# Optimization experiments

Measured on AMD Instinct MI355X. Metric: run time of the kernel, lower is better.

The kernel has to match this reference:

```python
import jax, jax.numpy as jnp
import numpy as np

N_NODES = 100_000
N_EDGES = 1_600_000
IN_DIM, HIDDEN, Z_DIM = 64, 128, 64


def _gcn_conv(x, src, dst, dinv, W, b, n):
    # PyG GCNConv: out_i = sum_j (d_i^-1/2 d_j^-1/2) (x_j @ W) + b, edges incl. self-loops
    xw = x @ W                                   # [N, out]
    norm = dinv[src] * dinv[dst]                 # [E+N]
    msg = xw[src] * norm[:, None]                # [E+N, out]
    return jax.ops.segment_sum(msg, dst, num_segments=n) + b


def _prep_graph(edge_index, n):
    loop = jnp.arange(n, dtype=edge_index.dtype)
    src = jnp.concatenate([edge_index[0], loop])
    dst = jnp.concatenate([edge_index[1], loop])
    deg = jax.ops.segment_sum(jnp.ones_like(dst, dtype=jnp.float32), dst, num_segments=n)
    dinv = jnp.where(deg > 0, jax.lax.rsqrt(jnp.maximum(deg, 1.0)), 0.0)
    return src, dst, dinv


def setup_inputs() -> dict:
    key = jax.random.key(0)
    ks = jax.random.split(key, 8)
    x = jax.random.normal(ks[0], (N_NODES, IN_DIM), dtype=jnp.float32)
    edge_index = jax.random.randint(ks[1], (2, N_EDGES), 0, N_NODES, dtype=jnp.int32)

    def glorot(k, fi, fo):
        s = (6.0 / (fi + fo)) ** 0.5
        return jax.random.uniform(k, (fi, fo), jnp.float32, -s, s)

    return {
        "x": x, "edge_index": edge_index,
        "W1": glorot(ks[2], IN_DIM, HIDDEN), "b1": jnp.zeros((HIDDEN,), jnp.float32),
        "W2": glorot(ks[3], HIDDEN, HIDDEN), "b2": jnp.zeros((HIDDEN,), jnp.float32),
        "Wmu": glorot(ks[4], HIDDEN, Z_DIM), "bmu": jnp.zeros((Z_DIM,), jnp.float32),
        "Wlv": glorot(ks[5], HIDDEN, Z_DIM), "blv": jnp.zeros((Z_DIM,), jnp.float32),
    }


def reference(x, edge_index, W1, b1, W2, b2, Wmu, bmu, Wlv, blv):
    n = x.shape[0]
    src, dst, dinv = _prep_graph(edge_index, n)
    h = jax.nn.relu(_gcn_conv(x, src, dst, dinv, W1, b1, n))
    h = jax.nn.relu(_gcn_conv(h, src, dst, dinv, W2, b2, n))
    # dropout p=0.0 (eval): identity
    mu = _gcn_conv(h, src, dst, dinv, Wmu, bmu, n)
    logvar = _gcn_conv(h, src, dst, dinv, Wlv, blv, n)
    return (mu, logvar)
```

## Files before the change

### kernel.cpp

```cpp
#include <hip/hip_runtime.h>
#include <hip/hip_fp16.h>
#include <cstddef>

#define N_NODES 100000
#define N_EDGES 1600000
#define E_TOT   (N_EDGES + N_NODES)
#define IN_DIM  64
#define HIDDEN  128
#define Z_DIM   64

#define BN 128
#define NB ((N_NODES + BN - 1) / BN)
#define NCH 128

using f16x8 = __attribute__((ext_vector_type(8))) _Float16;
using f32x4 = __attribute__((ext_vector_type(4))) float;


__global__ __launch_bounds__(256) void prep_k(const float* __restrict__ x, __half* __restrict__ x16,
                                              const float* __restrict__ W1, const float* __restrict__ W2,
                                              const float* __restrict__ Wmu, const float* __restrict__ Wlv,
                                              __half* __restrict__ W1t, __half* __restrict__ W2t,
                                              __half* __restrict__ Wht) {
    int i = blockIdx.x * 256 + threadIdx.x;
    const int CAST = N_NODES * IN_DIM / 8;
    if (i < CAST) {
        const float4* in4 = (const float4*)x;
        float4 a = in4[2 * i], b = in4[2 * i + 1];
        __half2 h0 = __floats2half2_rn(a.x, a.y);
        __half2 h1 = __floats2half2_rn(a.z, a.w);
        __half2 h2 = __floats2half2_rn(b.x, b.y);
        __half2 h3 = __floats2half2_rn(b.z, b.w);
        uint4 pk = make_uint4(*(unsigned*)&h0, *(unsigned*)&h1, *(unsigned*)&h2, *(unsigned*)&h3);
        ((uint4*)x16)[i] = pk;
        return;
    }
    int j = i - CAST;
    if (j < 128 * 64) {
        int col = j >> 6, k = j & 63;
        W1t[j] = __float2half(W1[k * 128 + col]);
        return;
    }
    int m = j - 128 * 64;
    if (m < 128 * 128) {
        int col = m >> 7, k = m & 127;
        W2t[m] = __float2half(W2[k * 128 + col]);
        return;
    }
    int h = m - 128 * 128;
    if (h < 128 * 128) {
        int col = h >> 7, k = h & 127;
        Wht[h] = __float2half(col < 64 ? Wmu[k * 64 + col] : Wlv[k * 64 + (col - 64)]);
    }
}


__global__ __launch_bounds__(256) void hist_k(const int* __restrict__ dst, int* __restrict__ histG, int e) {
    __shared__ int hist[NB];
    int c = blockIdx.x, t = threadIdx.x;
    int ch = (e + NCH - 1) / NCH;
    int i0 = c * ch, i1 = i0 + ch; if (i1 > e) i1 = e;
    for (int b = t; b < NB; b += 256) hist[b] = 0;
    __syncthreads();
    for (int i = i0 + t; i < i1; i += 256)
        atomicAdd(&hist[dst[i] >> 7], 1);
    __syncthreads();
    for (int b = t; b < NB; b += 256) histG[c * NB + b] = hist[b];
}

__global__ __launch_bounds__(1024) void boff_k(int* __restrict__ histG ,
                                               int* __restrict__ ebase, int e) {
    __shared__ int s[1024];
    int t = threadIdx.x;
    int run = 0;
    if (t < NB) {
        for (int c = 0; c < NCH; c++) {
            int v = histG[c * NB + t];
            histG[c * NB + t] = run;
            run += v;
        }
    }
    s[t] = (t < NB) ? run : 0;
    __syncthreads();
#pragma unroll
    for (int off = 1; off < 1024; off <<= 1) {
        int x = (t >= off) ? s[t - off] : 0;
        __syncthreads();
        s[t] += x;
        __syncthreads();
    }
    if (t < NB) ebase[t] = s[t] - run;
    if (t == 0) ebase[NB] = e;
}

__global__ __launch_bounds__(256) void binB_k(const int* __restrict__ src, const int* __restrict__ dst,
                                              const int* __restrict__ boffs, const int* __restrict__ ebase,
                                              int* __restrict__ binned, int e) {
    __shared__ int cur[NB];
    int c = blockIdx.x, t = threadIdx.x;
    int ch = (e + NCH - 1) / NCH;
    int i0 = c * ch, i1 = i0 + ch; if (i1 > e) i1 = e;
    for (int b = t; b < NB; b += 256) cur[b] = ebase[b] + boffs[c * NB + b];
    __syncthreads();
    for (int i = i0 + t; i < i1; i += 256) {
        int s = src[i], d = dst[i];
        int p = atomicAdd(&cur[d >> 7], 1);
        binned[p] = ((d & 127) << 17) | s;
    }
}

__global__ __launch_bounds__(256) void pdeg_k(const int* __restrict__ binned, const int* __restrict__ ebase,
                                              int* __restrict__ rowptr, float* __restrict__ dinv, int n) {
    __shared__ int hist[BN];
    __shared__ int sc[BN];
    int b = blockIdx.x, t = threadIdx.x;
    int n0 = b * BN;
    int nn = n - n0; if (nn > BN) nn = BN;
    if (t < BN) hist[t] = (t < nn) ? 1 : 0;
    __syncthreads();
    int e0 = ebase[b], e1 = ebase[b + 1];
    for (int i = e0 + t; i < e1; i += 256)
        atomicAdd(&hist[binned[i] >> 17], 1);
    __syncthreads();
    int v = (t < BN) ? hist[t] : 0;
    if (t < BN) sc[t] = v;
    __syncthreads();
#pragma unroll
    for (int off = 1; off < BN; off <<= 1) {
        int x = (t < BN && t >= off) ? sc[t - off] : 0;
        __syncthreads();
        if (t < BN) sc[t] += x;
        __syncthreads();
    }
    int base = e0 + n0;
    if (t < nn) {
        rowptr[n0 + t] = base + sc[t] - v;
        dinv[n0 + t] = rsqrtf((float)v);
    }
    if (b == gridDim.x - 1 && t == 0) rowptr[n] = E_TOT;
}

__global__ __launch_bounds__(256) void pfill_k(const int* __restrict__ binned, const int* __restrict__ ebase,
                                               const int* __restrict__ rowptr, const float* __restrict__ dinv,
                                               int2* __restrict__ em, int n) {
    __shared__ int cur[BN];
    __shared__ float sdv[BN];
    int b = blockIdx.x, t = threadIdx.x;
    int n0 = b * BN;
    int nn = n - n0; if (nn > BN) nn = BN;
    if (t < nn) {
        int rp = rowptr[n0 + t];
        float dv = dinv[n0 + t];
        sdv[t] = dv;
        em[rp] = make_int2(n0 + t, __float_as_int(dv * dv));
        cur[t] = rp + 1;
    }
    __syncthreads();
    int e0 = ebase[b], e1 = ebase[b + 1];
    for (int i = e0 + t; i < e1; i += 256) {
        int pk = binned[i];
        int ld = pk >> 17, s = pk & 0x1FFFF;
        int q = atomicAdd(&cur[ld], 1);
        em[q] = make_int2(s, __float_as_int(dinv[s] * sdv[ld]));
    }
}


template <int DIM, bool HEAD>
__global__ __launch_bounds__(256) void agg_k(const __half* __restrict__ H, const int* __restrict__ rowptr,
                                             const int2* __restrict__ em, __half* __restrict__ out,
                                             const float* __restrict__ bmu, const float* __restrict__ blv,
                                             float* __restrict__ mu, float* __restrict__ lv, int n) {
    int node = (int)((blockIdx.x * 256 + threadIdx.x) >> 6);
    if (node >= n) return;
    int lane = threadIdx.x & 63;
    int beg = rowptr[node], end = rowptr[node + 1];
    const uint4* H4 = (const uint4*)H;

    constexpr int RV   = DIM / 8;
    constexpr int SUBS = 64 / RV;
    constexpr int STEP = SUBS * 2;
    int sub = lane / RV;
    int fl  = lane % RV;

    float acc[8];
#pragma unroll
    for (int q = 0; q < 8; q++) acc[q] = 0.f;

    auto meta = [&](int j, int p, int& s, float& w) {
        int idx = j + SUBS * p + sub;
        int ci  = idx < end ? idx : beg;
        int2 e  = em[ci];
        s = e.x;
        w = idx < end ? __int_as_float(e.y) : 0.f;
    };
    auto rows = [&](int s0, int s1, uint4& r0, uint4& r1) {
        r0 = H4[(size_t)s0 * RV + fl];
        r1 = H4[(size_t)s1 * RV + fl];
    };
    auto fmas = [&](const uint4& r0, const uint4& r1, float ww0, float ww1) {
        const __half* h0 = (const __half*)&r0;
        const __half* h1 = (const __half*)&r1;
#pragma unroll
        for (int q = 0; q < 8; q++) acc[q] = fmaf(ww0, __half2float(h0[q]), acc[q]);
#pragma unroll
        for (int q = 0; q < 8; q++) acc[q] = fmaf(ww1, __half2float(h1[q]), acc[q]);
    };

    int G = (end - beg + STEP - 1) / STEP;

    int   sa0, sa1, sb0, sb1, sc0, sc1, sd0, sd1;
    float wa0, wa1, wb0, wb1, wc0, wc1, wd0, wd1;
    uint4 ra0, ra1, rb0, rb1, rc0, rc1, rd0, rd1;

    meta(beg,            0, sa0, wa0); meta(beg,            1, sa1, wa1);
    meta(beg + STEP,     0, sb0, wb0); meta(beg + STEP,     1, sb1, wb1);
    rows(sa0, sa1, ra0, ra1);
    rows(sb0, sb1, rb0, rb1);
    meta(beg + 2 * STEP, 0, sc0, wc0); meta(beg + 2 * STEP, 1, sc1, wc1);
    meta(beg + 3 * STEP, 0, sd0, wd0); meta(beg + 3 * STEP, 1, sd1, wd1);

    int g = 0;
    int jf = beg + 4 * STEP;
    while (true) {
        rows(sc0, sc1, rc0, rc1);
        fmas(ra0, ra1, wa0, wa1);
        if (++g >= G) break;
        meta(jf, 0, sa0, wa0); meta(jf, 1, sa1, wa1); jf += STEP;

        rows(sd0, sd1, rd0, rd1);
        fmas(rb0, rb1, wb0, wb1);
        if (++g >= G) break;
        meta(jf, 0, sb0, wb0); meta(jf, 1, sb1, wb1); jf += STEP;

        rows(sa0, sa1, ra0, ra1);
        fmas(rc0, rc1, wc0, wc1);
        if (++g >= G) break;
        meta(jf, 0, sc0, wc0); meta(jf, 1, sc1, wc1); jf += STEP;

        rows(sb0, sb1, rb0, rb1);
        fmas(rd0, rd1, wd0, wd1);
        if (++g >= G) break;
        meta(jf, 0, sd0, wd0); meta(jf, 1, sd1, wd1); jf += STEP;
    }

#pragma unroll
    for (int off = 32; off >= RV; off >>= 1) {
#pragma unroll
        for (int q = 0; q < 8; q++) acc[q] += __shfl_xor(acc[q], off);
    }
    if (sub == 0) {
        if constexpr (HEAD) {
            const float* bp = (fl < 8) ? (bmu + fl * 8) : (blv + (fl - 8) * 8);
#pragma unroll
            for (int q = 0; q < 8; q++) acc[q] += bp[q];
            float* op = (fl < 8) ? (mu + (size_t)node * 64 + fl * 8)
                                 : (lv + (size_t)node * 64 + (fl - 8) * 8);
            *(float4*)op = make_float4(acc[0], acc[1], acc[2], acc[3]);
            *(float4*)(op + 4) = make_float4(acc[4], acc[5], acc[6], acc[7]);
        } else {
            __half2 q0 = __floats2half2_rn(acc[0], acc[1]);
            __half2 q1 = __floats2half2_rn(acc[2], acc[3]);
            __half2 q2 = __floats2half2_rn(acc[4], acc[5]);
            __half2 q3 = __floats2half2_rn(acc[6], acc[7]);
            uint4 pk = make_uint4(*(unsigned*)&q0, *(unsigned*)&q1, *(unsigned*)&q2, *(unsigned*)&q3);
            *(uint4*)(out + (size_t)node * DIM + fl * 8) = pk;
        }
    }
}


template <int K, bool BR>
__global__ __launch_bounds__(256) void mgemm_k(const __half* __restrict__ A,
                                               const __half* __restrict__ Wt,
                                               const float* __restrict__ bias,
                                               __half* __restrict__ C, int n) {
    __shared__ __align__(16) __half Wl[128 * K];
    int t = threadIdx.x;

    constexpr int CHUNKS = 128 * K / 8;
    const uint4* Wg = (const uint4*)Wt;
    for (int i = t; i < CHUNKS; i += 256) {
        int g = i * 16;
        int col = g / (2 * K);
        uint4 v = Wg[i];
        *(uint4*)((char*)Wl + (g ^ ((col & 7) << 4))) = v;
    }
    __syncthreads();

    int lane = t & 63, w = t >> 6;
    int colb = lane & 15;
    int kq = (lane >> 4) * 8;
    int m0 = blockIdx.x * 64 + w * 16;
    int rowA = m0 + colb; if (rowA >= n) rowA = n - 1;
    const __half* Arow = A + (size_t)rowA * K + kq;

    f32x4 acc[8];
#pragma unroll
    for (int c = 0; c < 8; c++) acc[c] = (f32x4){0.f, 0.f, 0.f, 0.f};

    const char* wb = (const char*)Wl;
    int swz = (colb & 7) << 4;
    int off0 = colb * (2 * K) + kq * 2;

#pragma unroll
    for (int k0 = 0; k0 < K; k0 += 32) {
        f16x8 a = *(const f16x8*)(Arow + k0);
#pragma unroll
        for (int c = 0; c < 8; c++) {
            f16x8 b = *(const f16x8*)(wb + ((off0 + c * (32 * K) + k0 * 2) ^ swz));
            acc[c] = __builtin_amdgcn_mfma_f32_16x16x32_f16(a, b, acc[c], 0, 0, 0);
        }
    }

    int rbase = m0 + (lane >> 4) * 4;
#pragma unroll
    for (int c = 0; c < 8; c++) {
        int col = c * 16 + colb;
        float bv = BR ? bias[col] : 0.f;
#pragma unroll
        for (int r = 0; r < 4; r++) {
            int row = rbase + r;
            if (row < n) {
                float v = acc[c][r] + bv;
                if (BR) v = fmaxf(v, 0.f);
                C[(size_t)row * 128 + col] = __float2half(v);
            }
        }
    }
}


extern "C" void kernel_launch(void* const* d_in, const int* in_sizes, int n_in,
                              void* d_out, int out_size, void* d_ws, size_t ws_size,
                              hipStream_t stream) {
    const int N = N_NODES, E = N_EDGES, ETOT = E_TOT;

    const float* x    = (const float*)d_in[0];
    const int*   ei   = (const int*)d_in[1];
    const int*   srcA = ei;
    const int*   dstA = ei + E;
    const float* W1   = (const float*)d_in[2];
    const float* b1   = (const float*)d_in[3];
    const float* W2   = (const float*)d_in[4];
    const float* b2   = (const float*)d_in[5];
    const float* Wmu  = (const float*)d_in[6];
    const float* bmu  = (const float*)d_in[7];
    const float* Wlv  = (const float*)d_in[8];
    const float* blv  = (const float*)d_in[9];
    float* out = (float*)d_out;

    char* ws = (char*)d_ws;
    size_t o = 0;
    auto alloc = [&](size_t bytes) -> void* {
        o = (o + 255) & ~(size_t)255;
        void* p = ws + o;
        o += bytes;
        return p;
    };
    int*    histG  = (int*)alloc((size_t)NCH * NB * 4);
    int*    ebase  = (int*)alloc((size_t)(NB + 1) * 4);
    int*    rowptr = (int*)alloc((size_t)(N + 1) * 4);
    float*  dinv   = (float*)alloc((size_t)N * 4);
    int2*   em     = (int2*)alloc((size_t)ETOT * 8);
    int*    binned = (int*)alloc((size_t)E * 4);
    __half* x16    = (__half*)alloc((size_t)N * IN_DIM * 2);
    __half* B1     = (__half*)alloc((size_t)N * HIDDEN * 2);
    __half* B2     = (__half*)alloc((size_t)N * HIDDEN * 2);
    __half* W1t    = (__half*)alloc(128 * 64 * 2);
    __half* W2t    = (__half*)alloc(128 * 128 * 2);
    __half* Wht    = (__half*)alloc(128 * 128 * 2);
    (void)ws_size;

    const int PREP_T = N * IN_DIM / 8 + 128 * 64 + 128 * 128 + 128 * 128;
    const int gPrep = (PREP_T + 255) / 256;
    const int gAgg = (N + 3) / 4;
    const int gMg  = (N + 63) / 64;

    prep_k<<<gPrep, 256, 0, stream>>>(x, x16, W1, W2, Wmu, Wlv, W1t, W2t, Wht);
    hist_k<<<NCH, 256, 0, stream>>>(dstA, histG, E);
    boff_k<<<1, 1024, 0, stream>>>(histG, ebase, E);
    binB_k<<<NCH, 256, 0, stream>>>(srcA, dstA, histG, ebase, binned, E);
    pdeg_k<<<NB, 256, 0, stream>>>(binned, ebase, rowptr, dinv, N);
    pfill_k<<<NB, 256, 0, stream>>>(binned, ebase, rowptr, dinv, em, N);

    agg_k<64, false><<<gAgg, 256, 0, stream>>>(x16, rowptr, em, B1, nullptr, nullptr, nullptr, nullptr, N);
    mgemm_k<64, true><<<gMg, 256, 0, stream>>>(B1, W1t, b1, B2, N);

    agg_k<128, false><<<gAgg, 256, 0, stream>>>(B2, rowptr, em, B1, nullptr, nullptr, nullptr, nullptr, N);
    mgemm_k<128, true><<<gMg, 256, 0, stream>>>(B1, W2t, b2, B2, N);

    mgemm_k<128, false><<<gMg, 256, 0, stream>>>(B2, Wht, nullptr, B1, N);
    agg_k<128, true><<<gAgg, 256, 0, stream>>>(B1, rowptr, em, nullptr, bmu, blv,
                                               out, out + (size_t)N * Z_DIM, N);
}
```

Measured before the change: 369.8 us.

## Fuse histogram into prep kernel and parallelize bucket offset scan

Folds the per-chunk destination histogram into the prep/cast kernel as extra blocks, which removes one launch and lets the histogram run alongside the casting work. Doubles the chunk count to 256 so the histogram and binning passes have more parallelism. Replaces the serial per-bucket column scan, which ran in a single 1024-thread block, with a wave-per-bucket shuffle scan followed by a small block scan over bucket totals. The cost is one extra launch and a histogram buffer twice as large, and the prep blocks now reserve shared memory they do not use.

```diff
diff --git a/kernel.cpp b/kernel.cpp
--- a/kernel.cpp
+++ b/kernel.cpp
@@ -11,7 +11,7 @@
 
 #define BN 128
 #define NB ((N_NODES + BN - 1) / BN)
-#define NCH 128
+#define NCH 256
 
 using f16x8 = __attribute__((ext_vector_type(8))) _Float16;
 using f32x4 = __attribute__((ext_vector_type(4))) float;
@@ -21,8 +21,25 @@
                                               const float* __restrict__ W1, const float* __restrict__ W2,
                                               const float* __restrict__ Wmu, const float* __restrict__ Wlv,
                                               __half* __restrict__ W1t, __half* __restrict__ W2t,
-                                              __half* __restrict__ Wht) {
-    int i = blockIdx.x * 256 + threadIdx.x;
+                                              __half* __restrict__ Wht,
+                                              const int* __restrict__ dst, int* __restrict__ histG,
+                                              int e, int nPrep) {
+    __shared__ int hist[NB];
+    int blk = blockIdx.x;
+    int t = threadIdx.x;
+    if (blk >= nPrep) {
+        int c = blk - nPrep;
+        int ch = (e + NCH - 1) / NCH;
+        int i0 = c * ch, i1 = i0 + ch; if (i1 > e) i1 = e;
+        for (int b = t; b < NB; b += 256) hist[b] = 0;
+        __syncthreads();
+        for (int i = i0 + t; i < i1; i += 256)
+            atomicAdd(&hist[dst[i] >> 7], 1);
+        __syncthreads();
+        for (int b = t; b < NB; b += 256) histG[c * NB + b] = hist[b];
+        return;
+    }
+    int i = blk * 256 + t;
     const int CAST = N_NODES * IN_DIM / 8;
     if (i < CAST) {
         const float4* in4 = (const float4*)x;
@@ -55,32 +72,35 @@
 }
 
 
-__global__ __launch_bounds__(256) void hist_k(const int* __restrict__ dst, int* __restrict__ histG, int e) {
-    __shared__ int hist[NB];
-    int c = blockIdx.x, t = threadIdx.x;
-    int ch = (e + NCH - 1) / NCH;
-    int i0 = c * ch, i1 = i0 + ch; if (i1 > e) i1 = e;
-    for (int b = t; b < NB; b += 256) hist[b] = 0;
-    __syncthreads();
-    for (int i = i0 + t; i < i1; i += 256)
-        atomicAdd(&hist[dst[i] >> 7], 1);
-    __syncthreads();
-    for (int b = t; b < NB; b += 256) histG[c * NB + b] = hist[b];
-}
-
-__global__ __launch_bounds__(1024) void boff_k(int* __restrict__ histG ,
-                                               int* __restrict__ ebase, int e) {
+__global__ __launch_bounds__(256) void boffB_k(int* __restrict__ histG, int* __restrict__ btot) {
+    int wv = (int)((blockIdx.x * 256 + threadIdx.x) >> 6);
+    if (wv >= NB) return;
+    int lane = threadIdx.x & 63;
+    int v[4];
+#pragma unroll
+    for (int k = 0; k < 4; k++) v[k] = histG[(4 * lane + k) * NB + wv];
+    int s = v[0] + v[1] + v[2] + v[3];
+    int run = s;
+#pragma unroll
+    for (int off = 1; off < 64; off <<= 1) {
+        int tt = __shfl_up(run, off);
+        if (lane >= off) run += tt;
+    }
+    int p = run - s;
+#pragma unroll
+    for (int k = 0; k < 4; k++) {
+        int tt = v[k];
+        histG[(4 * lane + k) * NB + wv] = p;
+        p += tt;
+    }
+    if (lane == 63) btot[wv] = p;
+}
+
+__global__ __launch_bounds__(1024) void bscan_k(const int* __restrict__ btot, int* __restrict__ ebase, int e) {
     __shared__ int s[1024];
     int t = threadIdx.x;
-    int run = 0;
-    if (t < NB) {
-        for (int c = 0; c < NCH; c++) {
-            int v = histG[c * NB + t];
-            histG[c * NB + t] = run;
-            run += v;
-        }
-    }
-    s[t] = (t < NB) ? run : 0;
+    int v = (t < NB) ? btot[t] : 0;
+    s[t] = v;
     __syncthreads();
 #pragma unroll
     for (int off = 1; off < 1024; off <<= 1) {
@@ -89,7 +109,7 @@
         s[t] += x;
         __syncthreads();
     }
-    if (t < NB) ebase[t] = s[t] - run;
+    if (t < NB) ebase[t] = s[t] - v;
     if (t == 0) ebase[NB] = e;
 }
 
@@ -359,6 +379,7 @@
         return p;
     };
     int*    histG  = (int*)alloc((size_t)NCH * NB * 4);
+    int*    btot   = (int*)alloc((size_t)NB * 4);
     int*    ebase  = (int*)alloc((size_t)(NB + 1) * 4);
     int*    rowptr = (int*)alloc((size_t)(N + 1) * 4);
     float*  dinv   = (float*)alloc((size_t)N * 4);
@@ -373,13 +394,15 @@
     (void)ws_size;
 
     const int PREP_T = N * IN_DIM / 8 + 128 * 64 + 128 * 128 + 128 * 128;
-    const int gPrep = (PREP_T + 255) / 256;
+    const int nPrep = (PREP_T + 255) / 256;
     const int gAgg = (N + 3) / 4;
     const int gMg  = (N + 63) / 64;
-
-    prep_k<<<gPrep, 256, 0, stream>>>(x, x16, W1, W2, Wmu, Wlv, W1t, W2t, Wht);
-    hist_k<<<NCH, 256, 0, stream>>>(dstA, histG, E);
-    boff_k<<<1, 1024, 0, stream>>>(histG, ebase, E);
+    const int gBoff = (NB * 64 + 255) / 256;
+
+    prep_k<<<nPrep + NCH, 256, 0, stream>>>(x, x16, W1, W2, Wmu, Wlv, W1t, W2t, Wht,
+                                            dstA, histG, E, nPrep);
+    boffB_k<<<gBoff, 256, 0, stream>>>(histG, btot);
+    bscan_k<<<1, 1024, 0, stream>>>(btot, ebase, E);
     binB_k<<<NCH, 256, 0, stream>>>(srcA, dstA, histG, ebase, binned, E);
     pdeg_k<<<NB, 256, 0, stream>>>(binned, ebase, rowptr, dinv, N);
     pfill_k<<<NB, 256, 0, stream>>>(binned, ebase, rowptr, dinv, em, N);
```

Measured after the change: 359.7 us. 1.03x faster.
